# Kernel optimization log

Measured on AMD Instinct MI355X. Metric: run time of the kernel, lower is better.

## Reference

```python
import jax, jax.numpy as jnp
import numpy as np
from jax import lax

B, T, S, F = 16, 32, 128, 3
H = 256          # encoder_hidden = decoder_hidden = decoder_input
NH = 8           # n_head
TP = 4           # t_predict
DK = H // NH


def _lin(k, fan_in, shape):
    return jax.random.normal(k, shape, jnp.float32) * (1.0 / np.sqrt(fan_in))


def setup_inputs() -> dict:
    key = jax.random.key(0)
    ks = jax.random.split(key, 14)
    return {
        "input_data": jax.random.normal(ks[0], (B, T, S, F), jnp.float32),
        # encoder attention-LSTM cell (input_size=3)
        "enc_Wq": _lin(ks[1], H, (H, H)),
        "enc_Wk": _lin(ks[2], H, (H, H)),
        "enc_Wv": _lin(ks[3], H, (H, H)),
        "enc_Wg": _lin(ks[4], F + 2 * H, (F + 2 * H, 4 * H)),
        "enc_bg": jnp.zeros((4 * H,), jnp.float32),
        # decoder attention-LSTM cell (input_size=decoder_input=H)
        "dec_Wq": _lin(ks[5], H, (H, H)),
        "dec_Wk": _lin(ks[6], H, (H, H)),
        "dec_Wv": _lin(ks[7], H, (H, H)),
        "dec_Wg": _lin(ks[8], 3 * H, (3 * H, 4 * H)),
        "dec_bg": jnp.zeros((4 * H,), jnp.float32),
        # embedding Linear(encoder_hidden -> decoder_input)
        "emb_W": _lin(ks[9], H, (H, H)),
        "emb_b": jnp.zeros((H,), jnp.float32),
        # output Linear(decoder_hidden -> output_size=1)
        "out_W": _lin(ks[10], H, (H, 1)),
        "out_b": jnp.zeros((1,), jnp.float32),
    }


def spatial_hidden(h):
    # h: [B,S,H] -> [B,S,4,H] neighbors at offsets (+2,+1,-1,-2), zero-padded
    z1 = jnp.zeros_like(h[:, :1])
    z2 = jnp.zeros_like(h[:, :2])
    after1 = jnp.concatenate([h[:, 1:], z1], axis=1)
    before1 = jnp.concatenate([z1, h[:, :-1]], axis=1)
    after2 = jnp.concatenate([h[:, 2:], z2], axis=1)
    before2 = jnp.concatenate([z2, h[:, :-2]], axis=1)
    return jnp.stack([after2, after1, before1, before2], axis=2)


def attn_lstm_cell(x, h, c, sp, Wq, Wk, Wv, Wg, bg):
    # x:[B,S,Fin] h,c:[B,S,H] sp:[B,S,4,H]
    b, s, _ = h.shape
    q = (h @ Wq).reshape(b, s, NH, DK)
    k = (sp @ Wk).reshape(b, s, 4, NH, DK)
    v = (sp @ Wv).reshape(b, s, 4, NH, DK)
    scores = jnp.einsum('bshd,bsnhd->bshn', q, k) / np.sqrt(DK).astype(np.float32)
    attn = jax.nn.softmax(scores, axis=-1)
    ctx = jnp.einsum('bshn,bsnhd->bshd', attn, v).reshape(b, s, H)
    z = jnp.concatenate([x, h, ctx], axis=-1) @ Wg + bg
    i, f, g, o = jnp.split(z, 4, axis=-1)
    c_new = jax.nn.sigmoid(f) * c + jax.nn.sigmoid(i) * jnp.tanh(g)
    h_new = jax.nn.sigmoid(o) * jnp.tanh(c_new)
    return h_new, c_new


def reference(input_data, enc_Wq, enc_Wk, enc_Wv, enc_Wg, enc_bg,
              dec_Wq, dec_Wk, dec_Wv, dec_Wg, dec_bg,
              emb_W, emb_b, out_W, out_b):
    b, t, s, f = input_data.shape
    eh = jnp.zeros((b, s, H), input_data.dtype)
    ec = jnp.zeros((b, s, H), input_data.dtype)
    dh = jnp.zeros((b, s, H), input_data.dtype)

    cur = jnp.swapaxes(input_data[:, :-1], 0, 1)  # [T-1,B,S,F]
    nxt = jnp.swapaxes(input_data[:, 1:], 0, 1)   # [T-1,B,S,F]

    def step(carry, xt):
        eh, ec, dh = carry
        x_cur, x_nxt = xt
        esp = spatial_hidden(eh)
        dsp = spatial_hidden(dh)
        eh, ec = attn_lstm_cell(x_cur, eh, ec, esp, enc_Wq, enc_Wk, enc_Wv, enc_Wg, enc_bg)
        code = jax.nn.sigmoid(eh @ emb_W + emb_b)
        # NOTE: original code passes decoder_h as both h and c (decoder_c unused)
        dh, _ = attn_lstm_cell(code, dh, dh, dsp, dec_Wq, dec_Wk, dec_Wv, dec_Wg, dec_bg)
        out = dh @ out_W + out_b                                   # [B,S,1]
        In = jnp.concatenate([x_nxt[:, 0:1, 1:2], out[:, :-1, :]], axis=1)
        num = x_cur[:, :, 2:3] + In - out
        next_data = jnp.concatenate([out, In, num], axis=2)        # [B,S,3]
        return (eh, ec, dh), next_data

    _, outs = lax.scan(step, (eh, ec, dh), (cur, nxt))
    # keep only steps with time >= t_predict
    return jnp.swapaxes(outs[TP:], 0, 1)  # [B, T-TP-1, S, 3]
```

## Files before the change

### kernel.cpp

```cpp
#include <hip/hip_runtime.h>
#include <hip/hip_bf16.h>

#define Bz 16
#define Tz 32
#define Sz 128
#define TPz 4
#define Mz (Bz*Sz)
#define NSTEP (Tz-1)

typedef __bf16 bf16x8 __attribute__((ext_vector_type(8)));
typedef float  f32x4  __attribute__((ext_vector_type(4)));

#define MFMA __builtin_amdgcn_mfma_f32_16x16x32_bf16

__device__ __forceinline__ float sigf(float x) { return 1.f/(1.f + __expf(-x)); }

__global__ __launch_bounds__(256) void prep3(
    const float* __restrict__ encWq, const float* __restrict__ encWk,
    const float* __restrict__ encWv, const float* __restrict__ encWg,
    const float* __restrict__ decWq, const float* __restrict__ decWk,
    const float* __restrict__ decWv, const float* __restrict__ decWg,
    const float* __restrict__ embW,
    __bf16* __restrict__ Pqkv_e, __bf16* __restrict__ Pqkv_d,
    __bf16* __restrict__ Pemb,   __bf16* __restrict__ Pg_e,
    __bf16* __restrict__ Pg_d)
{
    int id = blockIdx.x * 256 + threadIdx.x;
    if (id < 768*256) {
        int f = id >> 9, e = id & 511, l = e >> 3, j = e & 7;
        int nt = f >> 3, kt = f & 7;
        int n = nt*16 + (l & 15), k = kt*32 + (l >> 4)*8 + j;
        float v = (n < 256) ? encWq[k*256 + n]
                : (n < 512) ? encWk[k*256 + (n-256)]
                            : encWv[k*256 + (n-512)];
        Pqkv_e[id] = (__bf16)v; return;
    }
    id -= 768*256;
    if (id < 768*256) {
        int f = id >> 9, e = id & 511, l = e >> 3, j = e & 7;
        int nt = f >> 3, kt = f & 7;
        int n = nt*16 + (l & 15), k = kt*32 + (l >> 4)*8 + j;
        float v = (n < 256) ? decWq[k*256 + n]
                : (n < 512) ? decWk[k*256 + (n-256)]
                            : decWv[k*256 + (n-512)];
        Pqkv_d[id] = (__bf16)v; return;
    }
    id -= 768*256;
    if (id < 256*256) {
        int f = id >> 9, e = id & 511, l = e >> 3, j = e & 7;
        int nt = f >> 3, kt = f & 7;
        int n = nt*16 + (l & 15), k = kt*32 + (l >> 4)*8 + j;
        Pemb[id] = (__bf16)embW[k*256 + n]; return;
    }
    id -= 256*256;
    if (id < 1024*512) {
        int f = id >> 9, e = id & 511, l = e >> 3, j = e & 7;
        int nt = f >> 4, kt = f & 15;
        int cht = nt >> 2, g = nt & 3;
        int ch = cht*16 + (l & 15), k = kt*32 + (l >> 4)*8 + j;
        Pg_e[id] = (__bf16)encWg[(size_t)(3 + k)*1024 + g*256 + ch]; return;
    }
    id -= 1024*512;
    if (id < 1024*768) {
        int f = id >> 9, e = id & 511, l = e >> 3, j = e & 7;
        int nt = f / 24, kt = f % 24;
        int cht = nt >> 2, g = nt & 3;
        int ch = cht*16 + (l & 15), k = kt*32 + (l >> 4)*8 + j;
        Pg_d[id] = (__bf16)decWg[(size_t)k*1024 + g*256 + ch]; return;
    }
}

__device__ __forceinline__ void qkv_lds(
    const __bf16* src264, const __bf16* __restrict__ P,
    __bf16* qL, __bf16* kvL, int tid)
{
    const int w = tid >> 6, lane = tid & 63, quad = (lane >> 4), lr = lane & 15;
    #pragma unroll
    for (int ng = 0; ng < 3; ++ng) {
        const int ntA = w*6 + ng*2;
        f32x4 acc[2][3];
        #pragma unroll
        for (int i = 0; i < 2; ++i)
            #pragma unroll
            for (int m = 0; m < 3; ++m) acc[i][m] = f32x4{0.f,0.f,0.f,0.f};
        for (int kt = 0; kt < 8; ++kt) {
            bf16x8 a0 = *(const bf16x8*)&src264[(lr)*264      + kt*32 + quad*8];
            bf16x8 a1 = *(const bf16x8*)&src264[(16 + lr)*264 + kt*32 + quad*8];
            bf16x8 a2 = *(const bf16x8*)&src264[(32 + lr)*264 + kt*32 + quad*8];
            bf16x8 b0 = *(const bf16x8*)&P[((size_t)(ntA*8 + kt)*64 + lane)*8];
            bf16x8 b1 = *(const bf16x8*)&P[((size_t)((ntA+1)*8 + kt)*64 + lane)*8];
            acc[0][0] = MFMA(a0, b0, acc[0][0], 0,0,0);
            acc[0][1] = MFMA(a1, b0, acc[0][1], 0,0,0);
            acc[0][2] = MFMA(a2, b0, acc[0][2], 0,0,0);
            acc[1][0] = MFMA(a0, b1, acc[1][0], 0,0,0);
            acc[1][1] = MFMA(a1, b1, acc[1][1], 0,0,0);
            acc[1][2] = MFMA(a2, b1, acc[1][2], 0,0,0);
        }
        #pragma unroll
        for (int i = 0; i < 2; ++i) {
            const int col = (ntA + i)*16 + lr;
            #pragma unroll
            for (int m = 0; m < 3; ++m)
                #pragma unroll
                for (int r = 0; r < 4; ++r) {
                    const int row = m*16 + quad*4 + r;
                    const float v = acc[i][m][r];
                    if (col < 256) {
                        if (row >= 2 && row < 34) qL[(row-2)*264 + col] = (__bf16)v;
                    } else if (row < 36) {
                        kvL[row*520 + (col - 256)] = (__bf16)v;
                    }
                }
        }
    }
}

__device__ __forceinline__ void attn_lds(
    const __bf16* qL, const __bf16* kvL, __bf16* cxL, int s0, int tid)
{
    const int w = tid >> 6, lane = tid & 63, quad = lane >> 4, lr = lane & 15;
    const int r = 4*w + quad, s = s0 + r, ch0 = lr*16;

    float q[16];
    {
        bf16x8 q0 = *(const bf16x8*)&qL[r*264 + ch0];
        bf16x8 q1 = *(const bf16x8*)&qL[r*264 + ch0 + 8];
        #pragma unroll
        for (int i = 0; i < 8; ++i) { q[i] = (float)q0[i]; q[8+i] = (float)q1[i]; }
    }
    bf16x8 zv;
    #pragma unroll
    for (int i = 0; i < 8; ++i) zv[i] = (__bf16)0.f;

    const int offs[4] = {2, 1, -1, -2};
    float sc[4]; bf16x8 v0[4], v1[4];
    #pragma unroll
    for (int n = 0; n < 4; ++n) {
        const int s2 = s + offs[n];
        const bool ok = ((unsigned)s2 < 128u);
        const int lrow = r + offs[n] + 2;
        float p = 0.f;
        if (ok) {
            bf16x8 k0 = *(const bf16x8*)&kvL[lrow*520 + ch0];
            bf16x8 k1 = *(const bf16x8*)&kvL[lrow*520 + ch0 + 8];
            v0[n] = *(const bf16x8*)&kvL[lrow*520 + 256 + ch0];
            v1[n] = *(const bf16x8*)&kvL[lrow*520 + 256 + ch0 + 8];
            #pragma unroll
            for (int i = 0; i < 8; ++i) p += q[i]*(float)k0[i] + q[8+i]*(float)k1[i];
        } else { v0[n] = zv; v1[n] = zv; }
        p += __shfl_xor(p, 1);
        sc[n] = ok ? p * 0.17677669529663687f : 0.f;
    }
    const float mx = fmaxf(fmaxf(sc[0], sc[1]), fmaxf(sc[2], sc[3]));
    float se = 0.f, aw[4];
    #pragma unroll
    for (int n = 0; n < 4; ++n) { aw[n] = __expf(sc[n] - mx); se += aw[n]; }
    const float inv = 1.f / se;
    float cx[16];
    #pragma unroll
    for (int i = 0; i < 16; ++i) cx[i] = 0.f;
    #pragma unroll
    for (int n = 0; n < 4; ++n)
        #pragma unroll
        for (int i = 0; i < 8; ++i) {
            cx[i]   += aw[n]*(float)v0[n][i];
            cx[8+i] += aw[n]*(float)v1[n][i];
        }
    bf16x8 o0, o1;
    #pragma unroll
    for (int i = 0; i < 8; ++i) { o0[i] = (__bf16)(cx[i]*inv); o1[i] = (__bf16)(cx[8+i]*inv); }
    *(bf16x8*)&cxL[r*264 + ch0]     = o0;
    *(bf16x8*)&cxL[r*264 + ch0 + 8] = o1;
}

__global__ __launch_bounds__(512, 2) void f_enc(
    const float* __restrict__ input, int t,
    const __bf16* __restrict__ Xp, __bf16* __restrict__ Xq,
    const __bf16* __restrict__ Pqkv_e, const __bf16* __restrict__ Pg_e,
    const float* __restrict__ encWg, const float* __restrict__ encbg,
    float* __restrict__ ec)
{
    __shared__ __attribute__((aligned(16))) __bf16 hL  [36*264];
    __shared__ __attribute__((aligned(16))) __bf16 kvL [36*520];
    __shared__ __attribute__((aligned(16))) __bf16 qL  [32*264];
    __shared__ __attribute__((aligned(16))) __bf16 cxL [32*264];
    __shared__ float xL[96];

    const int tid  = threadIdx.x;
    const int w    = tid >> 6;
    const int lane = tid & 63;
    const int quad = lane >> 4, lr = lane & 15;
    const int b    = blockIdx.x >> 4;
    const int rg   = (blockIdx.x >> 2) & 3;
    const int qt   = blockIdx.x & 3;
    const int gbatch = b*128, s0 = rg*32, grow0 = gbatch + s0;
    const int mt = w >> 2, ct = w & 3;
    const int ch = qt*64 + ct*16 + lr;

    for (int v = tid; v < 36*32; v += 512) {
        const int row = v >> 5, seg = v & 31, s = s0 - 2 + row;
        bf16x8 val;
        if ((unsigned)s < 128u)
            val = *(const bf16x8*)&Xp[(size_t)(gbatch + s)*512 + seg*8];
        else {
            #pragma unroll
            for (int i = 0; i < 8; ++i) val[i] = (__bf16)0.f;
        }
        *(bf16x8*)&hL[row*264 + seg*8] = val;
    }
    if (tid < 96) xL[tid] = input[((size_t)(b*Tz + t)*Sz + s0)*3 + tid];
    __syncthreads();

    qkv_lds(hL, Pqkv_e, qL, kvL, tid);
    __syncthreads();
    attn_lds(qL, kvL, cxL, s0, tid);
    __syncthreads();

    float wx0[4], wx1[4], wx2[4], bgv[4];
    #pragma unroll
    for (int g = 0; g < 4; ++g) {
        const int c = g*256 + ch;
        wx0[g] = encWg[c]; wx1[g] = encWg[1024 + c]; wx2[g] = encWg[2048 + c];
        bgv[g] = encbg[c];
    }
    f32x4 acc[4];
    #pragma unroll
    for (int g = 0; g < 4; ++g) acc[g] = f32x4{0.f,0.f,0.f,0.f};
    for (int kt = 0; kt < 16; ++kt) {
        const __bf16* As = (kt < 8)
            ? &hL [(2 + mt*16 + lr)*264 + kt*32 + quad*8]
            : &cxL[(mt*16 + lr)*264 + (kt-8)*32 + quad*8];
        bf16x8 af = *(const bf16x8*)As;
        #pragma unroll
        for (int g = 0; g < 4; ++g) {
            const int nt = qt*16 + ct*4 + g;
            bf16x8 bf = *(const bf16x8*)&Pg_e[((size_t)(nt*16 + kt)*64 + lane)*8];
            acc[g] = MFMA(af, bf, acc[g], 0,0,0);
        }
    }
    #pragma unroll
    for (int r = 0; r < 4; ++r) {
        const int row = mt*16 + quad*4 + r;
        const float x0 = xL[row*3], x1 = xL[row*3+1], x2 = xL[row*3+2];
        const float zi = acc[0][r] + x0*wx0[0] + x1*wx1[0] + x2*wx2[0] + bgv[0];
        const float zf = acc[1][r] + x0*wx0[1] + x1*wx1[1] + x2*wx2[1] + bgv[1];
        const float zg = acc[2][r] + x0*wx0[2] + x1*wx1[2] + x2*wx2[2] + bgv[2];
        const float zo = acc[3][r] + x0*wx0[3] + x1*wx1[3] + x2*wx2[3] + bgv[3];
        const size_t ei = (size_t)(grow0 + row)*256 + ch;
        const float cn = sigf(zf)*ec[ei] + sigf(zi)*tanhf(zg);
        ec[ei] = cn;
        Xq[(size_t)(grow0 + row)*512 + ch] = (__bf16)(sigf(zo)*tanhf(cn));
    }
}

__global__ __launch_bounds__(512, 2) void f_dec(
    const __bf16* __restrict__ Xp, __bf16* __restrict__ Xq,
    const __bf16* __restrict__ Pqkv_d, const __bf16* __restrict__ Pemb,
    const __bf16* __restrict__ Pg_d,
    const float* __restrict__ embb, const float* __restrict__ decbg,
    const float* __restrict__ outW, float* __restrict__ outbuf)
{
    __shared__ __attribute__((aligned(16))) __bf16 ehtL[32*264];
    __shared__ __attribute__((aligned(16))) __bf16 dhL [36*264];
    __shared__ __attribute__((aligned(16))) __bf16 kvL [36*520];
    __shared__ __attribute__((aligned(16))) __bf16 qL  [32*264];
    __shared__ __attribute__((aligned(16))) __bf16 cxL [32*264];
    __shared__ __attribute__((aligned(16))) __bf16 codeL[32*264];
    __shared__ float outredL[128];

    const int tid  = threadIdx.x;
    const int w    = tid >> 6;
    const int lane = tid & 63;
    const int quad = lane >> 4, lr = lane & 15;
    const int b    = blockIdx.x >> 4;
    const int rg   = (blockIdx.x >> 2) & 3;
    const int qt   = blockIdx.x & 3;
    const int gbatch = b*128, s0 = rg*32, grow0 = gbatch + s0;
    const int mt = w >> 2, ct = w & 3;
    const int ch = qt*64 + ct*16 + lr;

    for (int v = tid; v < 32*32; v += 512) {
        const int row = v >> 5, seg = v & 31;
        *(bf16x8*)&ehtL[row*264 + seg*8] =
            *(const bf16x8*)&Xq[(size_t)(grow0 + row)*512 + seg*8];
    }
    for (int v = tid; v < 36*32; v += 512) {
        const int row = v >> 5, seg = v & 31, s = s0 - 2 + row;
        bf16x8 val;
        if ((unsigned)s < 128u)
            val = *(const bf16x8*)&Xp[(size_t)(gbatch + s)*512 + 256 + seg*8];
        else {
            #pragma unroll
            for (int i = 0; i < 8; ++i) val[i] = (__bf16)0.f;
        }
        *(bf16x8*)&dhL[row*264 + seg*8] = val;
    }
    __syncthreads();

    {
        f32x4 cacc[2][2];
        #pragma unroll
        for (int m = 0; m < 2; ++m)
            #pragma unroll
            for (int i = 0; i < 2; ++i) cacc[m][i] = f32x4{0.f,0.f,0.f,0.f};
        for (int kt = 0; kt < 8; ++kt) {
            bf16x8 a0 = *(const bf16x8*)&ehtL[(lr)*264      + kt*32 + quad*8];
            bf16x8 a1 = *(const bf16x8*)&ehtL[(16 + lr)*264 + kt*32 + quad*8];
            #pragma unroll
            for (int i = 0; i < 2; ++i) {
                bf16x8 bf = *(const bf16x8*)&Pemb[((size_t)((2*w + i)*8 + kt)*64 + lane)*8];
                cacc[0][i] = MFMA(a0, bf, cacc[0][i], 0,0,0);
                cacc[1][i] = MFMA(a1, bf, cacc[1][i], 0,0,0);
            }
        }
        #pragma unroll
        for (int i = 0; i < 2; ++i) {
            const int col = (2*w + i)*16 + lr;
            const float bb = embb[col];
            #pragma unroll
            for (int m = 0; m < 2; ++m)
                #pragma unroll
                for (int r = 0; r < 4; ++r)
                    codeL[(m*16 + quad*4 + r)*264 + col] = (__bf16)sigf(cacc[m][i][r] + bb);
        }
    }
    qkv_lds(dhL, Pqkv_d, qL, kvL, tid);
    __syncthreads();
    attn_lds(qL, kvL, cxL, s0, tid);
    __syncthreads();

    float bgv[4];
    #pragma unroll
    for (int g = 0; g < 4; ++g) bgv[g] = decbg[g*256 + ch];
    const float ow = outW[ch];

    f32x4 acc[4];
    #pragma unroll
    for (int g = 0; g < 4; ++g) acc[g] = f32x4{0.f,0.f,0.f,0.f};
    for (int kt = 0; kt < 24; ++kt) {
        const __bf16* As = (kt < 8)
            ? &codeL[(mt*16 + lr)*264 + kt*32 + quad*8]
            : (kt < 16)
            ? &dhL[(2 + mt*16 + lr)*264 + (kt-8)*32 + quad*8]
            : &cxL[(mt*16 + lr)*264 + (kt-16)*32 + quad*8];
        bf16x8 af = *(const bf16x8*)As;
        #pragma unroll
        for (int g = 0; g < 4; ++g) {
            const int nt = qt*16 + ct*4 + g;
            bf16x8 bf = *(const bf16x8*)&Pg_d[((size_t)(nt*24 + kt)*64 + lane)*8];
            acc[g] = MFMA(af, bf, acc[g], 0,0,0);
        }
    }
    #pragma unroll
    for (int r = 0; r < 4; ++r) {
        const int row = mt*16 + quad*4 + r;
        const float zi = acc[0][r] + bgv[0];
        const float zf = acc[1][r] + bgv[1];
        const float zg = acc[2][r] + bgv[2];
        const float zo = acc[3][r] + bgv[3];
        const float c_old = (float)dhL[(2 + row)*264 + ch];
        const float cn = sigf(zf)*c_old + sigf(zi)*tanhf(zg);
        const float h  = sigf(zo)*tanhf(cn);
        Xq[(size_t)(grow0 + row)*512 + 256 + ch] = (__bf16)h;
        float pv = h * ow;
        pv += __shfl_xor(pv, 1); pv += __shfl_xor(pv, 2);
        pv += __shfl_xor(pv, 4); pv += __shfl_xor(pv, 8);
        if (lr == 0) outredL[row*4 + ct] = pv;
    }
    __syncthreads();
    if (tid < 32) {
        const float s4 = outredL[tid*4] + outredL[tid*4+1]
                       + outredL[tid*4+2] + outredL[tid*4+3];
        atomicAdd(&outbuf[grow0 + tid], s4);
    }
}

__global__ __launch_bounds__(256) void assemble_k(
    const float* __restrict__ outbuf, const float* __restrict__ input,
    const float* __restrict__ outb, float* __restrict__ out)
{
    const int idx = blockIdx.x*256 + threadIdx.x;
    const int NT = NSTEP - TPz;
    if (idx >= Bz*NT*Sz) return;
    const int s  = idx & 127;
    const int bi = idx >> 7;
    const int i  = bi % NT;
    const int b  = bi / NT;
    const int t  = i + TPz;
    const float ob = outb[0];
    const float o  = outbuf[t*Mz + (b<<7) + s] + ob;
    const float In = (s == 0)
        ? input[((size_t)(b*Tz + t + 1)*Sz)*3 + 1]
        : outbuf[t*Mz + (b<<7) + s - 1] + ob;
    const float num = input[((size_t)(b*Tz + t)*Sz + s)*3 + 2] + In - o;
    const size_t base = ((size_t)(b*NT + i)*Sz + s)*3;
    out[base+0] = o;
    out[base+1] = In;
    out[base+2] = num;
}

extern "C" void kernel_launch(void* const* d_in, const int* in_sizes, int n_in,
                              void* d_out, int out_size, void* d_ws, size_t ws_size,
                              hipStream_t stream)
{
    const float* input = (const float*)d_in[0];
    const float* encWq = (const float*)d_in[1];
    const float* encWk = (const float*)d_in[2];
    const float* encWv = (const float*)d_in[3];
    const float* encWg = (const float*)d_in[4];
    const float* encbg = (const float*)d_in[5];
    const float* decWq = (const float*)d_in[6];
    const float* decWk = (const float*)d_in[7];
    const float* decWv = (const float*)d_in[8];
    const float* decWg = (const float*)d_in[9];
    const float* decbg = (const float*)d_in[10];
    const float* embW  = (const float*)d_in[11];
    const float* embb  = (const float*)d_in[12];
    const float* outW  = (const float*)d_in[13];
    const float* outb  = (const float*)d_in[14];

    char* ws = (char*)d_ws;
    size_t off = 0;
    auto alloc = [&](size_t bytes) -> void* {
        void* p = ws + off;
        off += (bytes + 255) & ~(size_t)255;
        return p;
    };
    __bf16* Pqkv_e = (__bf16*)alloc((size_t)768*256*2);
    __bf16* Pqkv_d = (__bf16*)alloc((size_t)768*256*2);
    __bf16* Pemb   = (__bf16*)alloc((size_t)256*256*2);
    __bf16* Pg_e   = (__bf16*)alloc((size_t)1024*512*2);
    __bf16* Pg_d   = (__bf16*)alloc((size_t)1024*768*2);
    __bf16* Xa     = (__bf16*)alloc((size_t)Mz*512*2);
    __bf16* Xb     = (__bf16*)alloc((size_t)Mz*512*2);
    float*  ec     = (float*) alloc((size_t)Mz*256*4);
    float*  outbuf = (float*) alloc((size_t)NSTEP*Mz*4);

    hipMemsetAsync(Xa, 0, (size_t)Mz*512*2, stream);
    hipMemsetAsync(ec, 0, (size_t)Mz*256*4, stream);
    hipMemsetAsync(outbuf, 0, (size_t)NSTEP*Mz*4, stream);

    prep3<<<6912, 256, 0, stream>>>(encWq, encWk, encWv, encWg,
                                    decWq, decWk, decWv, decWg, embW,
                                    Pqkv_e, Pqkv_d, Pemb, Pg_e, Pg_d);

    for (int t = 0; t < NSTEP; ++t) {
        __bf16* Xp = (t & 1) ? Xb : Xa;
        __bf16* Xq = (t & 1) ? Xa : Xb;
        f_enc<<<256, 512, 0, stream>>>(input, t, Xp, Xq,
                                       Pqkv_e, Pg_e, encWg, encbg, ec);
        f_dec<<<256, 512, 0, stream>>>(Xp, Xq, Pqkv_d, Pemb, Pg_d,
                                       embb, decbg, outW, outbuf + t*Mz);
    }
    assemble_k<<<(Bz*(NSTEP-TPz)*Sz + 255)/256, 256, 0, stream>>>(
        outbuf, input, outb, (float*)d_out);
}
```

Before: 1.362 ms.

## Skew encoder and decoder steps into one fused per-step launch

The separate encoder and decoder kernels are merged into one kernel with 512 blocks. The first 256 blocks run decoder step k-1 and the last 256 run encoder step k, since the two only depend on earlier results. The two sides use disjoint column halves of the ping-pong buffers, and a shared char LDS arena is carved up per role. This halves the number of launches and lets the lighter encoder work overlap with decoder work. In exchange every block reserves the decoder's larger LDS footprint, which may limit how many blocks fit on each CU.

```diff
diff --git a/kernel.cpp b/kernel.cpp
--- a/kernel.cpp
+++ b/kernel.cpp
@@ -173,205 +173,207 @@
     *(bf16x8*)&cxL[r*264 + ch0 + 8] = o1;
 }
 
-__global__ __launch_bounds__(512, 2) void f_enc(
-    const float* __restrict__ input, int t,
-    const __bf16* __restrict__ Xp, __bf16* __restrict__ Xq,
-    const __bf16* __restrict__ Pqkv_e, const __bf16* __restrict__ Pg_e,
+#define SM_A264   0
+#define SM_KV     19008
+#define SM_Q      56448
+#define SM_CX     73344
+#define SM_EHT    90240
+#define SM_CODE   107136
+#define SM_MISC   124032
+#define SM_TOTAL  124544
+
+__global__ __launch_bounds__(512, 2) void step_k(
+    int k, const float* __restrict__ input,
+    __bf16* __restrict__ P, __bf16* __restrict__ Q,
+    const __bf16* __restrict__ Pqkv_e, const __bf16* __restrict__ Pqkv_d,
+    const __bf16* __restrict__ Pemb,   const __bf16* __restrict__ Pg_e,
+    const __bf16* __restrict__ Pg_d,
     const float* __restrict__ encWg, const float* __restrict__ encbg,
-    float* __restrict__ ec)
-{
-    __shared__ __attribute__((aligned(16))) __bf16 hL  [36*264];
-    __shared__ __attribute__((aligned(16))) __bf16 kvL [36*520];
-    __shared__ __attribute__((aligned(16))) __bf16 qL  [32*264];
-    __shared__ __attribute__((aligned(16))) __bf16 cxL [32*264];
-    __shared__ float xL[96];
+    const float* __restrict__ decbg, const float* __restrict__ embb,
+    const float* __restrict__ outW,
+    float* __restrict__ ec, float* __restrict__ outbuf)
+{
+    __shared__ __attribute__((aligned(16))) char SM[SM_TOTAL];
 
     const int tid  = threadIdx.x;
     const int w    = tid >> 6;
     const int lane = tid & 63;
     const int quad = lane >> 4, lr = lane & 15;
-    const int b    = blockIdx.x >> 4;
-    const int rg   = (blockIdx.x >> 2) & 3;
-    const int qt   = blockIdx.x & 3;
-    const int gbatch = b*128, s0 = rg*32, grow0 = gbatch + s0;
     const int mt = w >> 2, ct = w & 3;
-    const int ch = qt*64 + ct*16 + lr;
-
-    for (int v = tid; v < 36*32; v += 512) {
-        const int row = v >> 5, seg = v & 31, s = s0 - 2 + row;
-        bf16x8 val;
-        if ((unsigned)s < 128u)
-            val = *(const bf16x8*)&Xp[(size_t)(gbatch + s)*512 + seg*8];
-        else {
-            #pragma unroll
-            for (int i = 0; i < 8; ++i) val[i] = (__bf16)0.f;
-        }
-        *(bf16x8*)&hL[row*264 + seg*8] = val;
-    }
-    if (tid < 96) xL[tid] = input[((size_t)(b*Tz + t)*Sz + s0)*3 + tid];
-    __syncthreads();
-
-    qkv_lds(hL, Pqkv_e, qL, kvL, tid);
-    __syncthreads();
-    attn_lds(qL, kvL, cxL, s0, tid);
-    __syncthreads();
-
-    float wx0[4], wx1[4], wx2[4], bgv[4];
-    #pragma unroll
-    for (int g = 0; g < 4; ++g) {
-        const int c = g*256 + ch;
-        wx0[g] = encWg[c]; wx1[g] = encWg[1024 + c]; wx2[g] = encWg[2048 + c];
-        bgv[g] = encbg[c];
-    }
-    f32x4 acc[4];
-    #pragma unroll
-    for (int g = 0; g < 4; ++g) acc[g] = f32x4{0.f,0.f,0.f,0.f};
-    for (int kt = 0; kt < 16; ++kt) {
-        const __bf16* As = (kt < 8)
-            ? &hL [(2 + mt*16 + lr)*264 + kt*32 + quad*8]
-            : &cxL[(mt*16 + lr)*264 + (kt-8)*32 + quad*8];
-        bf16x8 af = *(const bf16x8*)As;
+
+    __bf16* hL   = (__bf16*)(SM + SM_A264);
+    __bf16* kvL  = (__bf16*)(SM + SM_KV);
+    __bf16* qL   = (__bf16*)(SM + SM_Q);
+    __bf16* cxL  = (__bf16*)(SM + SM_CX);
+
+    if (blockIdx.x >= 256) {
+        if (k >= NSTEP) return;
+        const int bid = blockIdx.x - 256;
+        const int b = bid >> 4, rg = (bid >> 2) & 3, qt = bid & 3;
+        const int gbatch = b*128, s0 = rg*32, grow0 = gbatch + s0;
+        const int ch = qt*64 + ct*16 + lr;
+        float* xL = (float*)(SM + SM_MISC);
+
+        for (int v = tid; v < 36*32; v += 512) {
+            const int row = v >> 5, seg = v & 31, s = s0 - 2 + row;
+            bf16x8 val;
+            if ((unsigned)s < 128u)
+                val = *(const bf16x8*)&P[(size_t)(gbatch + s)*512 + seg*8];
+            else {
+                #pragma unroll
+                for (int i = 0; i < 8; ++i) val[i] = (__bf16)0.f;
+            }
+            *(bf16x8*)&hL[row*264 + seg*8] = val;
+        }
+        if (tid < 96) xL[tid] = input[((size_t)(b*Tz + k)*Sz + s0)*3 + tid];
+        __syncthreads();
+
+        qkv_lds(hL, Pqkv_e, qL, kvL, tid);
+        __syncthreads();
+        attn_lds(qL, kvL, cxL, s0, tid);
+        __syncthreads();
+
+        float wx0[4], wx1[4], wx2[4], bgv[4];
         #pragma unroll
         for (int g = 0; g < 4; ++g) {
-            const int nt = qt*16 + ct*4 + g;
-            bf16x8 bf = *(const bf16x8*)&Pg_e[((size_t)(nt*16 + kt)*64 + lane)*8];
-            acc[g] = MFMA(af, bf, acc[g], 0,0,0);
-        }
-    }
-    #pragma unroll
-    for (int r = 0; r < 4; ++r) {
-        const int row = mt*16 + quad*4 + r;
-        const float x0 = xL[row*3], x1 = xL[row*3+1], x2 = xL[row*3+2];
-        const float zi = acc[0][r] + x0*wx0[0] + x1*wx1[0] + x2*wx2[0] + bgv[0];
-        const float zf = acc[1][r] + x0*wx0[1] + x1*wx1[1] + x2*wx2[1] + bgv[1];
-        const float zg = acc[2][r] + x0*wx0[2] + x1*wx1[2] + x2*wx2[2] + bgv[2];
-        const float zo = acc[3][r] + x0*wx0[3] + x1*wx1[3] + x2*wx2[3] + bgv[3];
-        const size_t ei = (size_t)(grow0 + row)*256 + ch;
-        const float cn = sigf(zf)*ec[ei] + sigf(zi)*tanhf(zg);
-        ec[ei] = cn;
-        Xq[(size_t)(grow0 + row)*512 + ch] = (__bf16)(sigf(zo)*tanhf(cn));
-    }
-}
-
-__global__ __launch_bounds__(512, 2) void f_dec(
-    const __bf16* __restrict__ Xp, __bf16* __restrict__ Xq,
-    const __bf16* __restrict__ Pqkv_d, const __bf16* __restrict__ Pemb,
-    const __bf16* __restrict__ Pg_d,
-    const float* __restrict__ embb, const float* __restrict__ decbg,
-    const float* __restrict__ outW, float* __restrict__ outbuf)
-{
-    __shared__ __attribute__((aligned(16))) __bf16 ehtL[32*264];
-    __shared__ __attribute__((aligned(16))) __bf16 dhL [36*264];
-    __shared__ __attribute__((aligned(16))) __bf16 kvL [36*520];
-    __shared__ __attribute__((aligned(16))) __bf16 qL  [32*264];
-    __shared__ __attribute__((aligned(16))) __bf16 cxL [32*264];
-    __shared__ __attribute__((aligned(16))) __bf16 codeL[32*264];
-    __shared__ float outredL[128];
-
-    const int tid  = threadIdx.x;
-    const int w    = tid >> 6;
-    const int lane = tid & 63;
-    const int quad = lane >> 4, lr = lane & 15;
-    const int b    = blockIdx.x >> 4;
-    const int rg   = (blockIdx.x >> 2) & 3;
-    const int qt   = blockIdx.x & 3;
-    const int gbatch = b*128, s0 = rg*32, grow0 = gbatch + s0;
-    const int mt = w >> 2, ct = w & 3;
-    const int ch = qt*64 + ct*16 + lr;
-
-    for (int v = tid; v < 32*32; v += 512) {
-        const int row = v >> 5, seg = v & 31;
-        *(bf16x8*)&ehtL[row*264 + seg*8] =
-            *(const bf16x8*)&Xq[(size_t)(grow0 + row)*512 + seg*8];
-    }
-    for (int v = tid; v < 36*32; v += 512) {
-        const int row = v >> 5, seg = v & 31, s = s0 - 2 + row;
-        bf16x8 val;
-        if ((unsigned)s < 128u)
-            val = *(const bf16x8*)&Xp[(size_t)(gbatch + s)*512 + 256 + seg*8];
-        else {
-            #pragma unroll
-            for (int i = 0; i < 8; ++i) val[i] = (__bf16)0.f;
-        }
-        *(bf16x8*)&dhL[row*264 + seg*8] = val;
-    }
-    __syncthreads();
-
-    {
-        f32x4 cacc[2][2];
-        #pragma unroll
-        for (int m = 0; m < 2; ++m)
-            #pragma unroll
-            for (int i = 0; i < 2; ++i) cacc[m][i] = f32x4{0.f,0.f,0.f,0.f};
-        for (int kt = 0; kt < 8; ++kt) {
-            bf16x8 a0 = *(const bf16x8*)&ehtL[(lr)*264      + kt*32 + quad*8];
-            bf16x8 a1 = *(const bf16x8*)&ehtL[(16 + lr)*264 + kt*32 + quad*8];
+            const int c = g*256 + ch;
+            wx0[g] = encWg[c]; wx1[g] = encWg[1024 + c]; wx2[g] = encWg[2048 + c];
+            bgv[g] = encbg[c];
+        }
+        f32x4 acc[4];
+        #pragma unroll
+        for (int g = 0; g < 4; ++g) acc[g] = f32x4{0.f,0.f,0.f,0.f};
+        for (int kt = 0; kt < 16; ++kt) {
+            const __bf16* As = (kt < 8)
+                ? &hL [(2 + mt*16 + lr)*264 + kt*32 + quad*8]
+                : &cxL[(mt*16 + lr)*264 + (kt-8)*32 + quad*8];
+            bf16x8 af = *(const bf16x8*)As;
+            #pragma unroll
+            for (int g = 0; g < 4; ++g) {
+                const int nt = qt*16 + ct*4 + g;
+                bf16x8 bf = *(const bf16x8*)&Pg_e[((size_t)(nt*16 + kt)*64 + lane)*8];
+                acc[g] = MFMA(af, bf, acc[g], 0,0,0);
+            }
+        }
+        #pragma unroll
+        for (int r = 0; r < 4; ++r) {
+            const int row = mt*16 + quad*4 + r;
+            const float x0 = xL[row*3], x1 = xL[row*3+1], x2 = xL[row*3+2];
+            const float zi = acc[0][r] + x0*wx0[0] + x1*wx1[0] + x2*wx2[0] + bgv[0];
+            const float zf = acc[1][r] + x0*wx0[1] + x1*wx1[1] + x2*wx2[1] + bgv[1];
+            const float zg = acc[2][r] + x0*wx0[2] + x1*wx1[2] + x2*wx2[2] + bgv[2];
+            const float zo = acc[3][r] + x0*wx0[3] + x1*wx1[3] + x2*wx2[3] + bgv[3];
+            const size_t ei = (size_t)(grow0 + row)*256 + ch;
+            const float cn = sigf(zf)*ec[ei] + sigf(zi)*tanhf(zg);
+            ec[ei] = cn;
+            Q[(size_t)(grow0 + row)*512 + ch] = (__bf16)(sigf(zo)*tanhf(cn));
+        }
+    } else {
+        if (k < 1) return;
+        const int td = k - 1;
+        const int bid = blockIdx.x;
+        const int b = bid >> 4, rg = (bid >> 2) & 3, qt = bid & 3;
+        const int gbatch = b*128, s0 = rg*32, grow0 = gbatch + s0;
+        const int ch = qt*64 + ct*16 + lr;
+        __bf16* dhL   = hL;
+        __bf16* ehtL  = (__bf16*)(SM + SM_EHT);
+        __bf16* codeL = (__bf16*)(SM + SM_CODE);
+        float* outredL = (float*)(SM + SM_MISC);
+
+        for (int v = tid; v < 32*32; v += 512) {
+            const int row = v >> 5, seg = v & 31;
+            *(bf16x8*)&ehtL[row*264 + seg*8] =
+                *(const bf16x8*)&P[(size_t)(grow0 + row)*512 + seg*8];
+        }
+        for (int v = tid; v < 36*32; v += 512) {
+            const int row = v >> 5, seg = v & 31, s = s0 - 2 + row;
+            bf16x8 val;
+            if ((unsigned)s < 128u)
+                val = *(const bf16x8*)&Q[(size_t)(gbatch + s)*512 + 256 + seg*8];
+            else {
+                #pragma unroll
+                for (int i = 0; i < 8; ++i) val[i] = (__bf16)0.f;
+            }
+            *(bf16x8*)&dhL[row*264 + seg*8] = val;
+        }
+        __syncthreads();
+
+        {
+            f32x4 cacc[2][2];
+            #pragma unroll
+            for (int m = 0; m < 2; ++m)
+                #pragma unroll
+                for (int i = 0; i < 2; ++i) cacc[m][i] = f32x4{0.f,0.f,0.f,0.f};
+            for (int kt = 0; kt < 8; ++kt) {
+                bf16x8 a0 = *(const bf16x8*)&ehtL[(lr)*264      + kt*32 + quad*8];
+                bf16x8 a1 = *(const bf16x8*)&ehtL[(16 + lr)*264 + kt*32 + quad*8];
+                #pragma unroll
+                for (int i = 0; i < 2; ++i) {
+                    bf16x8 bf = *(const bf16x8*)&Pemb[((size_t)((2*w + i)*8 + kt)*64 + lane)*8];
+                    cacc[0][i] = MFMA(a0, bf, cacc[0][i], 0,0,0);
+                    cacc[1][i] = MFMA(a1, bf, cacc[1][i], 0,0,0);
+                }
+            }
             #pragma unroll
             for (int i = 0; i < 2; ++i) {
-                bf16x8 bf = *(const bf16x8*)&Pemb[((size_t)((2*w + i)*8 + kt)*64 + lane)*8];
-                cacc[0][i] = MFMA(a0, bf, cacc[0][i], 0,0,0);
-                cacc[1][i] = MFMA(a1, bf, cacc[1][i], 0,0,0);
-            }
-        }
-        #pragma unroll
-        for (int i = 0; i < 2; ++i) {
-            const int col = (2*w + i)*16 + lr;
-            const float bb = embb[col];
-            #pragma unroll
-            for (int m = 0; m < 2; ++m)
-                #pragma unroll
-                for (int r = 0; r < 4; ++r)
-                    codeL[(m*16 + quad*4 + r)*264 + col] = (__bf16)sigf(cacc[m][i][r] + bb);
-        }
-    }
-    qkv_lds(dhL, Pqkv_d, qL, kvL, tid);
-    __syncthreads();
-    attn_lds(qL, kvL, cxL, s0, tid);
-    __syncthreads();
-
-    float bgv[4];
-    #pragma unroll
-    for (int g = 0; g < 4; ++g) bgv[g] = decbg[g*256 + ch];
-    const float ow = outW[ch];
-
-    f32x4 acc[4];
-    #pragma unroll
-    for (int g = 0; g < 4; ++g) acc[g] = f32x4{0.f,0.f,0.f,0.f};
-    for (int kt = 0; kt < 24; ++kt) {
-        const __bf16* As = (kt < 8)
-            ? &codeL[(mt*16 + lr)*264 + kt*32 + quad*8]
-            : (kt < 16)
-            ? &dhL[(2 + mt*16 + lr)*264 + (kt-8)*32 + quad*8]
-            : &cxL[(mt*16 + lr)*264 + (kt-16)*32 + quad*8];
-        bf16x8 af = *(const bf16x8*)As;
-        #pragma unroll
-        for (int g = 0; g < 4; ++g) {
-            const int nt = qt*16 + ct*4 + g;
-            bf16x8 bf = *(const bf16x8*)&Pg_d[((size_t)(nt*24 + kt)*64 + lane)*8];
-            acc[g] = MFMA(af, bf, acc[g], 0,0,0);
-        }
-    }
-    #pragma unroll
-    for (int r = 0; r < 4; ++r) {
-        const int row = mt*16 + quad*4 + r;
-        const float zi = acc[0][r] + bgv[0];
-        const float zf = acc[1][r] + bgv[1];
-        const float zg = acc[2][r] + bgv[2];
-        const float zo = acc[3][r] + bgv[3];
-        const float c_old = (float)dhL[(2 + row)*264 + ch];
-        const float cn = sigf(zf)*c_old + sigf(zi)*tanhf(zg);
-        const float h  = sigf(zo)*tanhf(cn);
-        Xq[(size_t)(grow0 + row)*512 + 256 + ch] = (__bf16)h;
-        float pv = h * ow;
-        pv += __shfl_xor(pv, 1); pv += __shfl_xor(pv, 2);
-        pv += __shfl_xor(pv, 4); pv += __shfl_xor(pv, 8);
-        if (lr == 0) outredL[row*4 + ct] = pv;
-    }
-    __syncthreads();
-    if (tid < 32) {
-        const float s4 = outredL[tid*4] + outredL[tid*4+1]
-                       + outredL[tid*4+2] + outredL[tid*4+3];
-        atomicAdd(&outbuf[grow0 + tid], s4);
+                const int col = (2*w + i)*16 + lr;
+                const float bb = embb[col];
+                #pragma unroll
+                for (int m = 0; m < 2; ++m)
+                    #pragma unroll
+                    for (int r = 0; r < 4; ++r)
+                        codeL[(m*16 + quad*4 + r)*264 + col] = (__bf16)sigf(cacc[m][i][r] + bb);
+            }
+        }
+        qkv_lds(dhL, Pqkv_d, qL, kvL, tid);
+        __syncthreads();
+        attn_lds(qL, kvL, cxL, s0, tid);
+        __syncthreads();
+
+        float bgv[4];
+        #pragma unroll
+        for (int g = 0; g < 4; ++g) bgv[g] = decbg[g*256 + ch];
+        const float ow = outW[ch];
+
+        f32x4 acc[4];
+        #pragma unroll
+        for (int g = 0; g < 4; ++g) acc[g] = f32x4{0.f,0.f,0.f,0.f};
+        for (int kt = 0; kt < 24; ++kt) {
+            const __bf16* As = (kt < 8)
+                ? &codeL[(mt*16 + lr)*264 + kt*32 + quad*8]
+                : (kt < 16)
+                ? &dhL[(2 + mt*16 + lr)*264 + (kt-8)*32 + quad*8]
+                : &cxL[(mt*16 + lr)*264 + (kt-16)*32 + quad*8];
+            bf16x8 af = *(const bf16x8*)As;
+            #pragma unroll
+            for (int g = 0; g < 4; ++g) {
+                const int nt = qt*16 + ct*4 + g;
+                bf16x8 bf = *(const bf16x8*)&Pg_d[((size_t)(nt*24 + kt)*64 + lane)*8];
+                acc[g] = MFMA(af, bf, acc[g], 0,0,0);
+            }
+        }
+        #pragma unroll
+        for (int r = 0; r < 4; ++r) {
+            const int row = mt*16 + quad*4 + r;
+            const float zi = acc[0][r] + bgv[0];
+            const float zf = acc[1][r] + bgv[1];
+            const float zg = acc[2][r] + bgv[2];
+            const float zo = acc[3][r] + bgv[3];
+            const float c_old = (float)dhL[(2 + row)*264 + ch];
+            const float cn = sigf(zf)*c_old + sigf(zi)*tanhf(zg);
+            const float h  = sigf(zo)*tanhf(cn);
+            P[(size_t)(grow0 + row)*512 + 256 + ch] = (__bf16)h;
+            float pv = h * ow;
+            pv += __shfl_xor(pv, 1); pv += __shfl_xor(pv, 2);
+            pv += __shfl_xor(pv, 4); pv += __shfl_xor(pv, 8);
+            if (lr == 0) outredL[row*4 + ct] = pv;
+        }
+        __syncthreads();
+        if (tid < 32) {
+            const float s4 = outredL[tid*4] + outredL[tid*4+1]
+                           + outredL[tid*4+2] + outredL[tid*4+3];
+            atomicAdd(&outbuf[(size_t)td*Mz + grow0 + tid], s4);
+        }
     }
 }
 
@@ -444,13 +446,13 @@
                                     decWq, decWk, decWv, decWg, embW,
                                     Pqkv_e, Pqkv_d, Pemb, Pg_e, Pg_d);
 
-    for (int t = 0; t < NSTEP; ++t) {
-        __bf16* Xp = (t & 1) ? Xb : Xa;
-        __bf16* Xq = (t & 1) ? Xa : Xb;
-        f_enc<<<256, 512, 0, stream>>>(input, t, Xp, Xq,
-                                       Pqkv_e, Pg_e, encWg, encbg, ec);
-        f_dec<<<256, 512, 0, stream>>>(Xp, Xq, Pqkv_d, Pemb, Pg_d,
-                                       embb, decbg, outW, outbuf + t*Mz);
+    for (int k = 0; k <= NSTEP; ++k) {
+        __bf16* P = (k & 1) ? Xb : Xa;
+        __bf16* Q = (k & 1) ? Xa : Xb;
+        step_k<<<512, 512, 0, stream>>>(k, input, P, Q,
+                                        Pqkv_e, Pqkv_d, Pemb, Pg_e, Pg_d,
+                                        encWg, encbg, decbg, embb, outW,
+                                        ec, outbuf);
     }
     assemble_k<<<(Bz*(NSTEP-TPz)*Sz + 255)/256, 256, 0, stream>>>(
         outbuf, input, outb, (float*)d_out);
```

Result: slower. 1.397 ms (+2.5%).
